# Optimization experiments

Hardware: AMD Instinct MI355X
Metric: run time of the kernel (lower is better)

The kernel has to match this reference:

```python
import jax, jax.numpy as jnp
import numpy as np

N, E = 50000, 800000
D_IN, HID, H, C, E_DIM = 128, 128, 4, 32, 32  # C = HID // H


def setup_inputs() -> dict:
    key = jax.random.key(0)
    ks = jax.random.split(key, 16)
    def lin(k, fan_in, fan_out):
        return jax.random.normal(k, (fan_in, fan_out), jnp.float32) / np.sqrt(fan_in)
    return {
        "x": jax.random.normal(ks[0], (N, D_IN), jnp.float32),
        "edge_index": jax.random.randint(ks[1], (2, E), 0, N, jnp.int32),
        "edge_attr": jax.random.normal(ks[2], (E, E_DIM), jnp.float32),
        # TransformerConv params (bias=True on q/k/v and skip; lin_edge has no bias in PyG)
        "Wq": lin(ks[3], D_IN, HID), "bq": jnp.zeros((HID,), jnp.float32),
        "Wk": lin(ks[4], D_IN, HID), "bk": jnp.zeros((HID,), jnp.float32),
        "Wv": lin(ks[5], D_IN, HID), "bv": jnp.zeros((HID,), jnp.float32),
        "We": lin(ks[6], E_DIM, HID),
        "Wskip": lin(ks[7], D_IN, HID), "bskip": jnp.zeros((HID,), jnp.float32),
        # MLP([HID, HID, HID]) -> two Linear layers, GELU(tanh) after each (plain_last=False)
        "W1": lin(ks[8], HID, HID), "b1": jnp.zeros((HID,), jnp.float32),
        "W2": lin(ks[9], HID, HID), "b2": jnp.zeros((HID,), jnp.float32),
    }


def reference(x, edge_index, edge_attr, Wq, bq, Wk, bk, Wv, bv, We, Wskip, bskip, W1, b1, W2, b2):
    src, dst = edge_index[0], edge_index[1]  # messages flow src(j) -> dst(i)
    n = x.shape[0]
    q = (x @ Wq + bq).reshape(n, H, C)
    k = (x @ Wk + bk).reshape(n, H, C)
    v = (x @ Wv + bv).reshape(n, H, C)
    e = (edge_attr @ We).reshape(-1, H, C)          # [E,H,C]
    kj = k[src] + e                                  # gather + edge lift
    vj = v[src] + e
    alpha = jnp.einsum("ehc,ehc->eh", q[dst], kj) / np.sqrt(C)  # [E,H]
    # segment softmax over destination neighborhoods (PyG softmax semantics)
    amax = jax.ops.segment_max(alpha, dst, num_segments=n)      # [N,H]
    amax = jnp.where(jnp.isfinite(amax), amax, 0.0)
    ex = jnp.exp(alpha - amax[dst])
    denom = jax.ops.segment_sum(ex, dst, num_segments=n)
    alpha = ex / (denom[dst] + 1e-16)
    # (attention dropout p=0.3 is inactive in eval mode)
    agg = jax.ops.segment_sum(vj * alpha[:, :, None], dst, num_segments=n)  # [N,H,C]
    out = agg.reshape(n, HID) + (x @ Wskip + bskip)  # concat heads + root skip
    # residual MLP: gelu(tanh) after every layer since plain_last=False, norm=None
    h = jax.nn.gelu(out @ W1 + b1, approximate=True)
    h = jax.nn.gelu(h @ W2 + b2, approximate=True)
    return out + h
```

## Files before the change

### kernel.cpp

```cpp
#include <hip/hip_runtime.h>
#include <math.h>


#define D 128
#define EDIM 32

using bf16x8 = __attribute__((ext_vector_type(8))) short;
using f32x4  = __attribute__((ext_vector_type(4))) float;
using ushort8 = __attribute__((ext_vector_type(8))) unsigned short;

__device__ inline unsigned short f2bf(float f) {
    unsigned int u = __float_as_uint(f);
    u += 0x7FFFu + ((u >> 16) & 1u);
    return (unsigned short)(u >> 16);
}
__device__ inline float bf2f(unsigned short h) {
    return __uint_as_float(((unsigned int)h) << 16);
}
__device__ inline float gelu_fast(float x) {
    float x3 = x * x * x;
    float u = 0.7978845608028654f * (x + 0.044715f * x3);
    float t = 1.f - 2.f / (__expf(2.f * u) + 1.f);
    return 0.5f * x * (1.f + t);
}
__device__ inline float quad_add(float x) {
    int a = __builtin_amdgcn_update_dpp(0, __float_as_int(x), 0xB1, 0xF, 0xF, true);
    x += __int_as_float(a);
    a = __builtin_amdgcn_update_dpp(0, __float_as_int(x), 0x4E, 0xF, 0xF, true);
    x += __int_as_float(a);
    return x;
}

__device__ inline bf16x8 ldsB(const unsigned short* sw, int col, int kk0) {
    return *(const bf16x8*)(sw + col * 128 + (kk0 ^ ((col & 7) << 3)));
}

__global__ __launch_bounds__(256) void prep_wt_hist(
    const float* __restrict__ Wq, const float* __restrict__ Wk,
    const float* __restrict__ Wv, const float* __restrict__ Wsk,
    const float* __restrict__ W1, const float* __restrict__ W2,
    const float* __restrict__ We, const float* __restrict__ bq,
    unsigned short* __restrict__ Wt, float* __restrict__ bqE,
    const int* __restrict__ EI, int* __restrict__ deg, int E)
{
    if (blockIdx.x >= 513) {
        int e = (blockIdx.x - 513) * 256 + threadIdx.x;
        if (e < E) atomicAdd(&deg[EI[E + e]], 1);
        return;
    }
    int t = blockIdx.x * 256 + threadIdx.x;
    int m = t >> 14;
    int r = t & 16383;
    if (m >= 8) {
        if (r < 128) {
            const int hb = r & 96, k = r & 31;
            const float* wek = We + (size_t)k * D + hb;
            float s = 0.f;
#pragma unroll 8
            for (int c = 0; c < 32; ++c) s = fmaf(bq[hb + c], wek[c], s);
            bqE[r] = s;
        }
        return;
    }
    int col = r & 127, kk = r >> 7;
    float v;
    if (m < 6) {
        const float* W = (m == 0) ? Wq : (m == 1) ? Wk : (m == 2) ? Wv
                       : (m == 3) ? Wsk : (m == 4) ? W1 : W2;
        v = W[(size_t)kk * D + col];
    } else if (m == 6) {
        const int hb = col & 96;
        const float* wqr = Wq + (size_t)kk * D + hb;
        const float* wer = We + (size_t)(col & 31) * D + hb;
        float s = 0.f;
#pragma unroll 8
        for (int c = 0; c < 32; ++c) s = fmaf(wqr[c], wer[c], s);
        v = s;
    } else {
        v = ((kk >> 5) == (col >> 5)) ? We[(size_t)(kk & 31) * D + col] : 0.f;
    }
    Wt[(size_t)m * 16384 + (size_t)col * 128 + (kk ^ ((col & 7) << 3))] = f2bf(v);
}

__global__ __launch_bounds__(1024) void scanA(
    const int* __restrict__ deg, int* __restrict__ rowptr,
    int* __restrict__ psums, int N)
{
    __shared__ int tmp[1024];
    const int t = threadIdx.x;
    const int i = blockIdx.x * 1024 + t;
    int v = (i < N) ? deg[i] : 0;
    tmp[t] = v;
    __syncthreads();
    for (int off = 1; off < 1024; off <<= 1) {
        int add = (t >= off) ? tmp[t - off] : 0;
        __syncthreads();
        tmp[t] += add;
        __syncthreads();
    }
    if (i < N) rowptr[i + 1] = tmp[t];
    if (t == 1023) psums[blockIdx.x] = tmp[1023];
}

__global__ __launch_bounds__(1024) void scanB(int* __restrict__ psums, int nb)
{
    __shared__ int tmp[1024];
    const int t = threadIdx.x;
    int v = (t < nb) ? psums[t] : 0;
    tmp[t] = v;
    __syncthreads();
    for (int off = 1; off < 1024; off <<= 1) {
        int add = (t >= off) ? tmp[t - off] : 0;
        __syncthreads();
        tmp[t] += add;
        __syncthreads();
    }
    if (t < nb) psums[t] = tmp[t] - v;
}

__global__ __launch_bounds__(256) void scanC(
    int* __restrict__ rowptr, int* __restrict__ cursor,
    const int* __restrict__ psums, int N)
{
    int i = blockIdx.x * 256 + threadIdx.x;
    if (i == 0) { rowptr[0] = 0; cursor[0] = 0; }
    if (i < N) {
        int val = rowptr[i + 1] + psums[i >> 10];
        rowptr[i + 1] = val;
        if (i + 1 < N) cursor[i + 1] = val;
    }
}

__global__ __launch_bounds__(256) void mega_scatter_gemm(
    const int* __restrict__ EI, const float* __restrict__ EA,
    int* __restrict__ cursor, int* __restrict__ srcs,
    unsigned short* __restrict__ EAP, int E, int EB,
    const float* __restrict__ x, const unsigned short* __restrict__ Wt,
    const float* __restrict__ bq, const float* __restrict__ bk,
    const float* __restrict__ bv, const float* __restrict__ bs,
    const float* __restrict__ bqE,
    unsigned short* __restrict__ QA, unsigned short* __restrict__ KV,
    float* __restrict__ S, int N, int NB)
{
    __shared__ unsigned short sw[16384];
    const int t = threadIdx.x;

    if ((int)blockIdx.x < EB) {
        int e = blockIdx.x * 256 + t;
        if (e >= E) return;
        int dst = EI[E + e];
        int pos = atomicAdd(&cursor[dst], 1);
        srcs[pos] = EI[e];
        const float4* s4 = (const float4*)(EA + (size_t)e * EDIM);
        unsigned short* op = EAP + (size_t)pos * EDIM;
#pragma unroll
        for (int j = 0; j < 4; ++j) {
            float4 a = s4[2 * j], b = s4[2 * j + 1];
            ushort8 u;
            u[0] = f2bf(a.x); u[1] = f2bf(a.y); u[2] = f2bf(a.z); u[3] = f2bf(a.w);
            u[4] = f2bf(b.x); u[5] = f2bf(b.y); u[6] = f2bf(b.z); u[7] = f2bf(b.w);
            *(ushort8*)(op + j * 8) = u;
        }
        return;
    }

    const int bid = blockIdx.x - EB;
    const int m = bid / NB;
    const int bx = bid - m * NB;
    const int widx = (m < 4) ? m : 6;
    const int lane = t & 63;
    const int w = t >> 6;
    const int row0 = bx * 64 + w * 16;
    const int lrow = lane & 15;
    const int kb = (lane >> 4) * 8;
    const int rq = (lane >> 4) * 4;

    const unsigned short* gsrc = Wt + (size_t)widx * 16384;
    ushort8 stg[8];
#pragma unroll
    for (int it = 0; it < 8; ++it)
        stg[it] = *(const ushort8*)(gsrc + (t + it * 256) * 8);

    bf16x8 af[4];
    {
        int ar = row0 + lrow; if (ar > N - 1) ar = N - 1;
        const float* xr = x + (size_t)ar * D + kb;
#pragma unroll
        for (int kf = 0; kf < 4; ++kf) {
            float4 p0 = *(const float4*)(xr + kf * 32);
            float4 p1 = *(const float4*)(xr + kf * 32 + 4);
            bf16x8 a;
            a[0] = (short)f2bf(p0.x); a[1] = (short)f2bf(p0.y);
            a[2] = (short)f2bf(p0.z); a[3] = (short)f2bf(p0.w);
            a[4] = (short)f2bf(p1.x); a[5] = (short)f2bf(p1.y);
            a[6] = (short)f2bf(p1.z); a[7] = (short)f2bf(p1.w);
            af[kf] = a;
        }
    }

#pragma unroll
    for (int it = 0; it < 8; ++it)
        *(ushort8*)(&sw[(t + it * 256) * 8]) = stg[it];
    __syncthreads();

    const float* bias = (m == 0) ? bq : (m == 1) ? bk : (m == 2) ? bv
                      : (m == 3) ? bs : bqE;
    f32x4 acc[8];
#pragma unroll
    for (int nf = 0; nf < 8; ++nf) acc[nf] = (f32x4){0.f, 0.f, 0.f, 0.f};
#pragma unroll
    for (int nf = 0; nf < 8; ++nf) {
        const int col = nf * 16 + lrow;
#pragma unroll
        for (int kf = 0; kf < 4; ++kf)
            acc[nf] = __builtin_amdgcn_mfma_f32_16x16x32_bf16(
                af[kf], ldsB(sw, col, kf * 32 + kb), acc[nf], 0, 0, 0);
    }
#pragma unroll
    for (int nf = 0; nf < 8; ++nf) {
        const int col = nf * 16 + lrow;
        const float bb = bias[col];
#pragma unroll
        for (int i = 0; i < 4; ++i) {
            int r = row0 + rq + i;
            if (r < N) {
                float v = acc[nf][i] + bb;
                if (m == 0)      QA[(size_t)r * 256 + col]       = f2bf(v);
                else if (m == 1) KV[(size_t)r * 256 + col]       = f2bf(v);
                else if (m == 2) KV[(size_t)r * 256 + 128 + col] = f2bf(v);
                else if (m == 3) S[(size_t)r * D + col]          = v;
                else             QA[(size_t)r * 256 + 128 + col] = f2bf(v);
            }
        }
    }
}

__global__ __launch_bounds__(256) void gather_pass(
    const int* __restrict__ rowptr, const int* __restrict__ srcs,
    const unsigned short* __restrict__ EAP,
    const unsigned short* __restrict__ QA, const unsigned short* __restrict__ KV,
    float* __restrict__ SB, unsigned short* __restrict__ SAS, int N)
{
    const int lane = threadIdx.x & 63;
    const int wid = threadIdx.x >> 6;
    const int n = blockIdx.x * 4 + wid;
    if (n >= N) return;
    const int g = lane & 15;
    const int grp = lane >> 4;
    const int eoff = (g & 3) * 8;

    float q8[8], qe8[8];
    {
        const unsigned short* qa = QA + (size_t)n * 256 + g * 8;
        bf16x8 qb  = *(const bf16x8*)(qa);
        bf16x8 qeb = *(const bf16x8*)(qa + 128);
#pragma unroll
        for (int j = 0; j < 8; ++j) {
            q8[j]  = bf2f((unsigned short)qb[j]);
            qe8[j] = bf2f((unsigned short)qeb[j]);
        }
    }

    float acc[8], sa[8], den = 0.f;
#pragma unroll
    for (int j = 0; j < 8; ++j) { acc[j] = 0.f; sa[j] = 0.f; }

    const int i0 = rowptr[n], i1 = rowptr[n + 1];

    int iA = i0 + grp, iB = iA + 4;
    int sA = (iA < i1) ? srcs[iA] : -1;
    int sB = (iB < i1) ? srcs[iB] : -1;

    for (int b = i0; b < i1; b += 8) {
        const int iA2 = iA + 8, iB2 = iB + 8;
        const int sA2 = (iA2 < i1) ? srcs[iA2] : -1;
        const int sB2 = (iB2 < i1) ? srcs[iB2] : -1;

        bf16x8 kA = {0,0,0,0,0,0,0,0}, vA = kA, eA = kA;
        bf16x8 kB = kA, vB = kA, eB = kA;
        if (sA >= 0) {
            const unsigned short* kv = KV + (size_t)sA * 256 + g * 8;
            kA = *(const bf16x8*)(kv);
            vA = *(const bf16x8*)(kv + 128);
            eA = *(const bf16x8*)(EAP + (size_t)iA * EDIM + eoff);
        }
        if (sB >= 0) {
            const unsigned short* kv = KV + (size_t)sB * 256 + g * 8;
            kB = *(const bf16x8*)(kv);
            vB = *(const bf16x8*)(kv + 128);
            eB = *(const bf16x8*)(EAP + (size_t)iB * EDIM + eoff);
        }

        {
            float ef[8];
            float p = 0.f;
#pragma unroll
            for (int j = 0; j < 8; ++j) {
                ef[j] = bf2f((unsigned short)eA[j]);
                p = fmaf(q8[j], bf2f((unsigned short)kA[j]),
                         fmaf(ef[j], qe8[j], p));
            }
            p = quad_add(p);
            const float ex = (sA >= 0) ? __expf(p * 0.17677669529663689f) : 0.f;
            den += ex;
#pragma unroll
            for (int j = 0; j < 8; ++j) {
                acc[j] = fmaf(ex, bf2f((unsigned short)vA[j]), acc[j]);
                sa[j]  = fmaf(ex, ef[j], sa[j]);
            }
        }
        {
            float ef[8];
            float p = 0.f;
#pragma unroll
            for (int j = 0; j < 8; ++j) {
                ef[j] = bf2f((unsigned short)eB[j]);
                p = fmaf(q8[j], bf2f((unsigned short)kB[j]),
                         fmaf(ef[j], qe8[j], p));
            }
            p = quad_add(p);
            const float ex = (sB >= 0) ? __expf(p * 0.17677669529663689f) : 0.f;
            den += ex;
#pragma unroll
            for (int j = 0; j < 8; ++j) {
                acc[j] = fmaf(ex, bf2f((unsigned short)vB[j]), acc[j]);
                sa[j]  = fmaf(ex, ef[j], sa[j]);
            }
        }
        iA = iA2; iB = iB2; sA = sA2; sB = sB2;
    }

#pragma unroll
    for (int off = 16; off <= 32; off <<= 1) {
        den += __shfl_xor(den, off, 64);
#pragma unroll
        for (int j = 0; j < 8; ++j) {
            acc[j] += __shfl_xor(acc[j], off, 64);
            sa[j]  += __shfl_xor(sa[j],  off, 64);
        }
    }

    if (grp == 0) {
        const float rden = 1.f / (den + 1e-16f);
        float* so = SB + (size_t)n * D + g * 8;
        unsigned short* po = SAS + (size_t)n * D + g * 8;
#pragma unroll
        for (int j = 0; j < 8; ++j) {
            so[j] = fmaf(acc[j], rden, so[j]);
            po[j] = f2bf(sa[j] * rden);
        }
    }
}

__global__ __launch_bounds__(256) void fused_mlp(
    const float* __restrict__ SB, const unsigned short* __restrict__ SAS,
    const unsigned short* __restrict__ WtC, const unsigned short* __restrict__ Wt1,
    const unsigned short* __restrict__ Wt2,
    const float* __restrict__ b1, const float* __restrict__ b2,
    float* __restrict__ FINAL, int N)
{
    __shared__ unsigned short sw[16384];
    __shared__ unsigned short bounce[64 * 136];
    const int t = threadIdx.x;
    const int lane = t & 63;
    const int w = t >> 6;
    const int row0 = blockIdx.x * 64 + w * 16;
    const int lrow = lane & 15;
    const int kb = (lane >> 4) * 8;
    const int rq = (lane >> 4) * 4;

    ushort8 stg[8];
#pragma unroll
    for (int it = 0; it < 8; ++it)
        stg[it] = *(const ushort8*)(WtC + (t + it * 256) * 8);

    bf16x8 af[4];
    {
        int ar = row0 + lrow; if (ar > N - 1) ar = N - 1;
        const unsigned short* xr = SAS + (size_t)ar * D + kb;
#pragma unroll
        for (int kf = 0; kf < 4; ++kf) af[kf] = *(const bf16x8*)(xr + kf * 32);
    }
    f32x4 out[8];
#pragma unroll
    for (int nf = 0; nf < 8; ++nf) {
        const int col = nf * 16 + lrow;
#pragma unroll
        for (int i = 0; i < 4; ++i) {
            int r = row0 + rq + i;
            out[nf][i] = (r < N) ? SB[(size_t)r * D + col] : 0.f;
        }
    }
#pragma unroll
    for (int it = 0; it < 8; ++it)
        *(ushort8*)(&sw[(t + it * 256) * 8]) = stg[it];
    __syncthreads();

#pragma unroll
    for (int nf = 0; nf < 8; ++nf) {
        const int col = nf * 16 + lrow;
#pragma unroll
        for (int kf = 0; kf < 4; ++kf)
            out[nf] = __builtin_amdgcn_mfma_f32_16x16x32_bf16(
                af[kf], ldsB(sw, col, kf * 32 + kb), out[nf], 0, 0, 0);
    }
    __syncthreads();

#pragma unroll
    for (int it = 0; it < 8; ++it)
        stg[it] = *(const ushort8*)(Wt1 + (t + it * 256) * 8);
#pragma unroll
    for (int nf = 0; nf < 8; ++nf) {
        const int col = nf * 16 + lrow;
#pragma unroll
        for (int i = 0; i < 4; ++i)
            bounce[(w * 16 + rq + i) * 136 + col] = f2bf(out[nf][i]);
    }
#pragma unroll
    for (int it = 0; it < 8; ++it)
        *(ushort8*)(&sw[(t + it * 256) * 8]) = stg[it];
    __syncthreads();

    bf16x8 af2[4];
#pragma unroll
    for (int kf = 0; kf < 4; ++kf)
        af2[kf] = *(const bf16x8*)(&bounce[(w * 16 + lrow) * 136 + kb + kf * 32]);
    f32x4 acc2[8];
#pragma unroll
    for (int nf = 0; nf < 8; ++nf) acc2[nf] = (f32x4){0.f, 0.f, 0.f, 0.f};
#pragma unroll
    for (int nf = 0; nf < 8; ++nf) {
        const int col = nf * 16 + lrow;
#pragma unroll
        for (int kf = 0; kf < 4; ++kf)
            acc2[nf] = __builtin_amdgcn_mfma_f32_16x16x32_bf16(
                af2[kf], ldsB(sw, col, kf * 32 + kb), acc2[nf], 0, 0, 0);
    }
    __syncthreads();

#pragma unroll
    for (int it = 0; it < 8; ++it)
        stg[it] = *(const ushort8*)(Wt2 + (t + it * 256) * 8);
#pragma unroll
    for (int nf = 0; nf < 8; ++nf) {
        const int col = nf * 16 + lrow;
        const float bb = b1[col];
#pragma unroll
        for (int i = 0; i < 4; ++i)
            bounce[(w * 16 + rq + i) * 136 + col] = f2bf(gelu_fast(acc2[nf][i] + bb));
    }
#pragma unroll
    for (int it = 0; it < 8; ++it)
        *(ushort8*)(&sw[(t + it * 256) * 8]) = stg[it];
    __syncthreads();

    bf16x8 af3[4];
#pragma unroll
    for (int kf = 0; kf < 4; ++kf)
        af3[kf] = *(const bf16x8*)(&bounce[(w * 16 + lrow) * 136 + kb + kf * 32]);
    f32x4 acc3[8];
#pragma unroll
    for (int nf = 0; nf < 8; ++nf) acc3[nf] = (f32x4){0.f, 0.f, 0.f, 0.f};
#pragma unroll
    for (int nf = 0; nf < 8; ++nf) {
        const int col = nf * 16 + lrow;
#pragma unroll
        for (int kf = 0; kf < 4; ++kf)
            acc3[nf] = __builtin_amdgcn_mfma_f32_16x16x32_bf16(
                af3[kf], ldsB(sw, col, kf * 32 + kb), acc3[nf], 0, 0, 0);
    }
#pragma unroll
    for (int nf = 0; nf < 8; ++nf) {
        const int col = nf * 16 + lrow;
        const float bb = b2[col];
#pragma unroll
        for (int i = 0; i < 4; ++i) {
            int r = row0 + rq + i;
            if (r < N)
                FINAL[(size_t)r * D + col] = out[nf][i] + gelu_fast(acc3[nf][i] + bb);
        }
    }
}

extern "C" void kernel_launch(void* const* d_in, const int* in_sizes, int n_in,
                              void* d_out, int out_size, void* d_ws, size_t ws_size,
                              hipStream_t stream)
{
    const float* x   = (const float*)d_in[0];
    const int*   EI  = (const int*)  d_in[1];
    const float* EA  = (const float*)d_in[2];
    const float* Wq  = (const float*)d_in[3];
    const float* bq  = (const float*)d_in[4];
    const float* Wk  = (const float*)d_in[5];
    const float* bk  = (const float*)d_in[6];
    const float* Wv  = (const float*)d_in[7];
    const float* bv  = (const float*)d_in[8];
    const float* We  = (const float*)d_in[9];
    const float* Wsk = (const float*)d_in[10];
    const float* bsk = (const float*)d_in[11];
    const float* W1  = (const float*)d_in[12];
    const float* b1  = (const float*)d_in[13];
    const float* W2  = (const float*)d_in[14];
    const float* b2  = (const float*)d_in[15];

    const int N = in_sizes[0] / D;
    const int E = in_sizes[1] / 2;

    char* p = (char*)d_ws;
    auto alloc = [&](size_t bytes) -> void* {
        void* r = (void*)p;
        p += (bytes + 255) & ~(size_t)255;
        return r;
    };
    float*          Sb     = (float*)         alloc((size_t)N * D * 4);
    unsigned short* QAb    = (unsigned short*)alloc((size_t)N * 256 * 2);
    unsigned short* KVb    = (unsigned short*)alloc((size_t)N * 256 * 2);
    unsigned short* SASb   = (unsigned short*)alloc((size_t)N * D * 2);
    unsigned short* EAPb   = (unsigned short*)alloc((size_t)E * EDIM * 2);
    int*            srcsb  = (int*)           alloc((size_t)E * 4);
    unsigned short* Wt     = (unsigned short*)alloc((size_t)8 * 16384 * 2);
    float*          bqEb   = (float*)         alloc((size_t)128 * 4);
    int*            deg    = (int*)           alloc((size_t)N * 4);
    int*            rowptr = (int*)           alloc((size_t)(N + 1) * 4);
    int*            cursor = (int*)           alloc((size_t)(N + 1) * 4);
    int*            psums  = (int*)           alloc((size_t)1024 * 4);

    hipMemsetAsync(deg, 0, (size_t)N * sizeof(int), stream);

    const int NB = (N + 63) / 64;
    const int EB = (E + 255) / 256;
    const int SB_ = (N + 1023) / 1024;

    prep_wt_hist<<<513 + EB, 256, 0, stream>>>(Wq, Wk, Wv, Wsk, W1, W2, We, bq,
                                               Wt, bqEb, EI, deg, E);

    scanA<<<SB_, 1024, 0, stream>>>(deg, rowptr, psums, N);
    scanB<<<1, 1024, 0, stream>>>(psums, SB_);
    scanC<<<(N + 255) / 256, 256, 0, stream>>>(rowptr, cursor, psums, N);

    mega_scatter_gemm<<<EB + 5 * NB, 256, 0, stream>>>(
        EI, EA, cursor, srcsb, EAPb, E, EB,
        x, Wt, bq, bk, bv, bsk, bqEb, QAb, KVb, Sb, N, NB);

    gather_pass<<<(N + 3) / 4, 256, 0, stream>>>(
        rowptr, srcsb, EAPb, QAb, KVb, Sb, SASb, N);

    fused_mlp<<<NB, 256, 0, stream>>>(Sb, SASb,
                                      Wt + (size_t)7 * 16384,
                                      Wt + (size_t)4 * 16384,
                                      Wt + (size_t)5 * 16384,
                                      b1, b2, (float*)d_out, N);
}
```

Before: 270.3 us.

## Gather edge attributes by original index and pre-convert x to bf16

The scatter phase no longer copies and bf16-converts edge attributes into CSR order. It now stores (src, edge id) pairs, and gather_pass reads fp32 edge_attr directly by original edge index. x is converted to bf16 once in the prep kernel, and each projection GEMM block now covers 128 rows with two MFMA accumulator sets sharing each B fragment. This removes a large edge-attribute write and reread pass, but makes the gather read fp32 attributes at random locations, doubling the bytes per edge there, and raises register use in the GEMM.

```diff
diff --git a/kernel.cpp b/kernel.cpp
--- a/kernel.cpp
+++ b/kernel.cpp
@@ -35,14 +35,27 @@
     return *(const bf16x8*)(sw + col * 128 + (kk0 ^ ((col & 7) << 3)));
 }
 
-__global__ __launch_bounds__(256) void prep_wt_hist(
+__global__ __launch_bounds__(256) void prep_kernel(
     const float* __restrict__ Wq, const float* __restrict__ Wk,
     const float* __restrict__ Wv, const float* __restrict__ Wsk,
     const float* __restrict__ W1, const float* __restrict__ W2,
     const float* __restrict__ We, const float* __restrict__ bq,
     unsigned short* __restrict__ Wt, float* __restrict__ bqE,
-    const int* __restrict__ EI, int* __restrict__ deg, int E)
-{
+    const int* __restrict__ EI, int* __restrict__ deg, int E, int HB,
+    const float* __restrict__ x, unsigned short* __restrict__ XB, long xtot)
+{
+    if ((int)blockIdx.x >= 513 + HB) {
+        long i8 = ((long)(blockIdx.x - 513 - HB) * 256 + threadIdx.x) * 8;
+        if (i8 + 8 <= xtot) {
+            float4 a = *(const float4*)(x + i8);
+            float4 b = *(const float4*)(x + i8 + 4);
+            ushort8 u;
+            u[0] = f2bf(a.x); u[1] = f2bf(a.y); u[2] = f2bf(a.z); u[3] = f2bf(a.w);
+            u[4] = f2bf(b.x); u[5] = f2bf(b.y); u[6] = f2bf(b.z); u[7] = f2bf(b.w);
+            *(ushort8*)(XB + i8) = u;
+        }
+        return;
+    }
     if (blockIdx.x >= 513) {
         int e = (blockIdx.x - 513) * 256 + threadIdx.x;
         if (e < E) atomicAdd(&deg[EI[E + e]], 1);
@@ -131,46 +144,36 @@
     }
 }
 
-__global__ __launch_bounds__(256) void mega_scatter_gemm(
-    const int* __restrict__ EI, const float* __restrict__ EA,
-    int* __restrict__ cursor, int* __restrict__ srcs,
-    unsigned short* __restrict__ EAP, int E, int EB,
-    const float* __restrict__ x, const unsigned short* __restrict__ Wt,
+__global__ __launch_bounds__(256) void mega_gemm_scatter(
+    const unsigned short* __restrict__ XB, const unsigned short* __restrict__ Wt,
     const float* __restrict__ bq, const float* __restrict__ bk,
     const float* __restrict__ bv, const float* __restrict__ bs,
     const float* __restrict__ bqE,
     unsigned short* __restrict__ QA, unsigned short* __restrict__ KV,
-    float* __restrict__ S, int N, int NB)
+    float* __restrict__ S, int N, int NB2,
+    const int* __restrict__ EI, int* __restrict__ cursor,
+    int2* __restrict__ SE, int E)
 {
     __shared__ unsigned short sw[16384];
     const int t = threadIdx.x;
 
-    if ((int)blockIdx.x < EB) {
-        int e = blockIdx.x * 256 + t;
-        if (e >= E) return;
-        int dst = EI[E + e];
-        int pos = atomicAdd(&cursor[dst], 1);
-        srcs[pos] = EI[e];
-        const float4* s4 = (const float4*)(EA + (size_t)e * EDIM);
-        unsigned short* op = EAP + (size_t)pos * EDIM;
-#pragma unroll
-        for (int j = 0; j < 4; ++j) {
-            float4 a = s4[2 * j], b = s4[2 * j + 1];
-            ushort8 u;
-            u[0] = f2bf(a.x); u[1] = f2bf(a.y); u[2] = f2bf(a.z); u[3] = f2bf(a.w);
-            u[4] = f2bf(b.x); u[5] = f2bf(b.y); u[6] = f2bf(b.z); u[7] = f2bf(b.w);
-            *(ushort8*)(op + j * 8) = u;
+    if ((int)blockIdx.x >= 5 * NB2) {
+        int e = (blockIdx.x - 5 * NB2) * 256 + t;
+        if (e < E) {
+            int dst = EI[E + e];
+            int pos = atomicAdd(&cursor[dst], 1);
+            SE[pos] = make_int2(EI[e], e);
         }
         return;
     }
 
-    const int bid = blockIdx.x - EB;
-    const int m = bid / NB;
-    const int bx = bid - m * NB;
+    const int bid = blockIdx.x;
+    const int m = bid / NB2;
+    const int bx = bid - m * NB2;
     const int widx = (m < 4) ? m : 6;
     const int lane = t & 63;
     const int w = t >> 6;
-    const int row0 = bx * 64 + w * 16;
+    const int row0 = bx * 128 + w * 32;
     const int lrow = lane & 15;
     const int kb = (lane >> 4) * 8;
     const int rq = (lane >> 4) * 4;
@@ -181,20 +184,16 @@
     for (int it = 0; it < 8; ++it)
         stg[it] = *(const ushort8*)(gsrc + (t + it * 256) * 8);
 
-    bf16x8 af[4];
+    bf16x8 af0[4], af1[4];
     {
-        int ar = row0 + lrow; if (ar > N - 1) ar = N - 1;
-        const float* xr = x + (size_t)ar * D + kb;
+        int a0 = row0 + lrow;      if (a0 > N - 1) a0 = N - 1;
+        int a1 = row0 + 16 + lrow; if (a1 > N - 1) a1 = N - 1;
+        const unsigned short* x0 = XB + (size_t)a0 * D + kb;
+        const unsigned short* x1 = XB + (size_t)a1 * D + kb;
 #pragma unroll
         for (int kf = 0; kf < 4; ++kf) {
-            float4 p0 = *(const float4*)(xr + kf * 32);
-            float4 p1 = *(const float4*)(xr + kf * 32 + 4);
-            bf16x8 a;
-            a[0] = (short)f2bf(p0.x); a[1] = (short)f2bf(p0.y);
-            a[2] = (short)f2bf(p0.z); a[3] = (short)f2bf(p0.w);
-            a[4] = (short)f2bf(p1.x); a[5] = (short)f2bf(p1.y);
-            a[6] = (short)f2bf(p1.z); a[7] = (short)f2bf(p1.w);
-            af[kf] = a;
+            af0[kf] = *(const bf16x8*)(x0 + kf * 32);
+            af1[kf] = *(const bf16x8*)(x1 + kf * 32);
         }
     }
 
@@ -205,39 +204,47 @@
 
     const float* bias = (m == 0) ? bq : (m == 1) ? bk : (m == 2) ? bv
                       : (m == 3) ? bs : bqE;
-    f32x4 acc[8];
-#pragma unroll
-    for (int nf = 0; nf < 8; ++nf) acc[nf] = (f32x4){0.f, 0.f, 0.f, 0.f};
-#pragma unroll
-    for (int nf = 0; nf < 8; ++nf) {
-        const int col = nf * 16 + lrow;
-#pragma unroll
-        for (int kf = 0; kf < 4; ++kf)
-            acc[nf] = __builtin_amdgcn_mfma_f32_16x16x32_bf16(
-                af[kf], ldsB(sw, col, kf * 32 + kb), acc[nf], 0, 0, 0);
-    }
-#pragma unroll
-    for (int nf = 0; nf < 8; ++nf) {
-        const int col = nf * 16 + lrow;
-        const float bb = bias[col];
-#pragma unroll
-        for (int i = 0; i < 4; ++i) {
-            int r = row0 + rq + i;
-            if (r < N) {
-                float v = acc[nf][i] + bb;
-                if (m == 0)      QA[(size_t)r * 256 + col]       = f2bf(v);
-                else if (m == 1) KV[(size_t)r * 256 + col]       = f2bf(v);
-                else if (m == 2) KV[(size_t)r * 256 + 128 + col] = f2bf(v);
-                else if (m == 3) S[(size_t)r * D + col]          = v;
-                else             QA[(size_t)r * 256 + 128 + col] = f2bf(v);
+    f32x4 acc0[8], acc1[8];
+#pragma unroll
+    for (int nf = 0; nf < 8; ++nf) {
+        acc0[nf] = (f32x4){0.f, 0.f, 0.f, 0.f};
+        acc1[nf] = (f32x4){0.f, 0.f, 0.f, 0.f};
+    }
+#pragma unroll
+    for (int nf = 0; nf < 8; ++nf) {
+        const int col = nf * 16 + lrow;
+#pragma unroll
+        for (int kf = 0; kf < 4; ++kf) {
+            bf16x8 bfr = ldsB(sw, col, kf * 32 + kb);
+            acc0[nf] = __builtin_amdgcn_mfma_f32_16x16x32_bf16(af0[kf], bfr, acc0[nf], 0, 0, 0);
+            acc1[nf] = __builtin_amdgcn_mfma_f32_16x16x32_bf16(af1[kf], bfr, acc1[nf], 0, 0, 0);
+        }
+    }
+#pragma unroll
+    for (int rb = 0; rb < 2; ++rb) {
+#pragma unroll
+        for (int nf = 0; nf < 8; ++nf) {
+            const int col = nf * 16 + lrow;
+            const float bb = bias[col];
+#pragma unroll
+            for (int i = 0; i < 4; ++i) {
+                int r = row0 + rb * 16 + rq + i;
+                if (r < N) {
+                    float v = ((rb == 0) ? acc0[nf][i] : acc1[nf][i]) + bb;
+                    if (m == 0)      QA[(size_t)r * 256 + col]       = f2bf(v);
+                    else if (m == 1) KV[(size_t)r * 256 + col]       = f2bf(v);
+                    else if (m == 2) KV[(size_t)r * 256 + 128 + col] = f2bf(v);
+                    else if (m == 3) S[(size_t)r * D + col]          = v;
+                    else             QA[(size_t)r * 256 + 128 + col] = f2bf(v);
+                }
             }
         }
     }
 }
 
 __global__ __launch_bounds__(256) void gather_pass(
-    const int* __restrict__ rowptr, const int* __restrict__ srcs,
-    const unsigned short* __restrict__ EAP,
+    const int* __restrict__ rowptr, const int2* __restrict__ SE,
+    const float* __restrict__ EA,
     const unsigned short* __restrict__ QA, const unsigned short* __restrict__ KV,
     float* __restrict__ SB, unsigned short* __restrict__ SAS, int N)
 {
@@ -268,40 +275,43 @@
     const int i0 = rowptr[n], i1 = rowptr[n + 1];
 
     int iA = i0 + grp, iB = iA + 4;
-    int sA = (iA < i1) ? srcs[iA] : -1;
-    int sB = (iB < i1) ? srcs[iB] : -1;
+    int2 seA = (iA < i1) ? SE[iA] : make_int2(-1, 0);
+    int2 seB = (iB < i1) ? SE[iB] : make_int2(-1, 0);
 
     for (int b = i0; b < i1; b += 8) {
         const int iA2 = iA + 8, iB2 = iB + 8;
-        const int sA2 = (iA2 < i1) ? srcs[iA2] : -1;
-        const int sB2 = (iB2 < i1) ? srcs[iB2] : -1;
-
-        bf16x8 kA = {0,0,0,0,0,0,0,0}, vA = kA, eA = kA;
-        bf16x8 kB = kA, vB = kA, eB = kA;
-        if (sA >= 0) {
-            const unsigned short* kv = KV + (size_t)sA * 256 + g * 8;
+        const int2 seA2 = (iA2 < i1) ? SE[iA2] : make_int2(-1, 0);
+        const int2 seB2 = (iB2 < i1) ? SE[iB2] : make_int2(-1, 0);
+
+        bf16x8 kA = {0,0,0,0,0,0,0,0}, vA = kA;
+        bf16x8 kB = kA, vB = kA;
+        float4 eA0 = {0,0,0,0}, eA1 = eA0, eB0 = eA0, eB1 = eA0;
+        if (seA.x >= 0) {
+            const unsigned short* kv = KV + (size_t)seA.x * 256 + g * 8;
             kA = *(const bf16x8*)(kv);
             vA = *(const bf16x8*)(kv + 128);
-            eA = *(const bf16x8*)(EAP + (size_t)iA * EDIM + eoff);
-        }
-        if (sB >= 0) {
-            const unsigned short* kv = KV + (size_t)sB * 256 + g * 8;
+            const float* ear = EA + (size_t)seA.y * EDIM + eoff;
+            eA0 = *(const float4*)(ear);
+            eA1 = *(const float4*)(ear + 4);
+        }
+        if (seB.x >= 0) {
+            const unsigned short* kv = KV + (size_t)seB.x * 256 + g * 8;
             kB = *(const bf16x8*)(kv);
             vB = *(const bf16x8*)(kv + 128);
-            eB = *(const bf16x8*)(EAP + (size_t)iB * EDIM + eoff);
+            const float* ear = EA + (size_t)seB.y * EDIM + eoff;
+            eB0 = *(const float4*)(ear);
+            eB1 = *(const float4*)(ear + 4);
         }
 
         {
-            float ef[8];
+            float ef[8] = {eA0.x, eA0.y, eA0.z, eA0.w, eA1.x, eA1.y, eA1.z, eA1.w};
             float p = 0.f;
 #pragma unroll
-            for (int j = 0; j < 8; ++j) {
-                ef[j] = bf2f((unsigned short)eA[j]);
+            for (int j = 0; j < 8; ++j)
                 p = fmaf(q8[j], bf2f((unsigned short)kA[j]),
                          fmaf(ef[j], qe8[j], p));
-            }
             p = quad_add(p);
-            const float ex = (sA >= 0) ? __expf(p * 0.17677669529663689f) : 0.f;
+            const float ex = (seA.x >= 0) ? __expf(p * 0.17677669529663689f) : 0.f;
             den += ex;
 #pragma unroll
             for (int j = 0; j < 8; ++j) {
@@ -310,16 +320,14 @@
             }
         }
         {
-            float ef[8];
+            float ef[8] = {eB0.x, eB0.y, eB0.z, eB0.w, eB1.x, eB1.y, eB1.z, eB1.w};
             float p = 0.f;
 #pragma unroll
-            for (int j = 0; j < 8; ++j) {
-                ef[j] = bf2f((unsigned short)eB[j]);
+            for (int j = 0; j < 8; ++j)
                 p = fmaf(q8[j], bf2f((unsigned short)kB[j]),
                          fmaf(ef[j], qe8[j], p));
-            }
             p = quad_add(p);
-            const float ex = (sB >= 0) ? __expf(p * 0.17677669529663689f) : 0.f;
+            const float ex = (seB.x >= 0) ? __expf(p * 0.17677669529663689f) : 0.f;
             den += ex;
 #pragma unroll
             for (int j = 0; j < 8; ++j) {
@@ -327,7 +335,7 @@
                 sa[j]  = fmaf(ex, ef[j], sa[j]);
             }
         }
-        iA = iA2; iB = iB2; sA = sA2; sB = sB2;
+        iA = iA2; iB = iB2; seA = seA2; seB = seB2;
     }
 
 #pragma unroll
@@ -516,8 +524,8 @@
     unsigned short* QAb    = (unsigned short*)alloc((size_t)N * 256 * 2);
     unsigned short* KVb    = (unsigned short*)alloc((size_t)N * 256 * 2);
     unsigned short* SASb   = (unsigned short*)alloc((size_t)N * D * 2);
-    unsigned short* EAPb   = (unsigned short*)alloc((size_t)E * EDIM * 2);
-    int*            srcsb  = (int*)           alloc((size_t)E * 4);
+    unsigned short* XBb    = (unsigned short*)alloc((size_t)N * D * 2);
+    int2*           SEb    = (int2*)          alloc((size_t)E * 8);
     unsigned short* Wt     = (unsigned short*)alloc((size_t)8 * 16384 * 2);
     float*          bqEb   = (float*)         alloc((size_t)128 * 4);
     int*            deg    = (int*)           alloc((size_t)N * 4);
@@ -527,23 +535,26 @@
 
     hipMemsetAsync(deg, 0, (size_t)N * sizeof(int), stream);
 
-    const int NB = (N + 63) / 64;
-    const int EB = (E + 255) / 256;
+    const long xtot = (long)N * D;
+    const int NB  = (N + 63) / 64;
+    const int NB2 = (N + 127) / 128;
+    const int EB  = (E + 255) / 256;
+    const int XB_ = (int)((xtot + 2047) / 2048);
     const int SB_ = (N + 1023) / 1024;
 
-    prep_wt_hist<<<513 + EB, 256, 0, stream>>>(Wq, Wk, Wv, Wsk, W1, W2, We, bq,
-                                               Wt, bqEb, EI, deg, E);
+    prep_kernel<<<513 + EB + XB_, 256, 0, stream>>>(
+        Wq, Wk, Wv, Wsk, W1, W2, We, bq, Wt, bqEb, EI, deg, E, EB, x, XBb, xtot);
 
     scanA<<<SB_, 1024, 0, stream>>>(deg, rowptr, psums, N);
     scanB<<<1, 1024, 0, stream>>>(psums, SB_);
     scanC<<<(N + 255) / 256, 256, 0, stream>>>(rowptr, cursor, psums, N);
 
-    mega_scatter_gemm<<<EB + 5 * NB, 256, 0, stream>>>(
-        EI, EA, cursor, srcsb, EAPb, E, EB,
-        x, Wt, bq, bk, bv, bsk, bqEb, QAb, KVb, Sb, N, NB);
+    mega_gemm_scatter<<<5 * NB2 + EB, 256, 0, stream>>>(
+        XBb, Wt, bq, bk, bv, bsk, bqEb, QAb, KVb, Sb, N, NB2,
+        EI, cursor, SEb, E);
 
     gather_pass<<<(N + 3) / 4, 256, 0, stream>>>(
-        rowptr, srcsb, EAPb, QAb, KVb, Sb, SASb, N);
+        rowptr, SEb, EA, QAb, KVb, Sb, SASb, N);
 
     fused_mlp<<<NB, 256, 0, stream>>>(Sb, SASb,
                                       Wt + (size_t)7 * 16384,
```

Measured after the change: 279.7 us. +3.5%, slower.
